# Performance work log

Measured on AMD Instinct MI355X. Metric: run time of the kernel, lower is better.

Reference implementation:

```python
import jax, jax.numpy as jnp
import numpy as np
import math

B, S, HID = 4, 1024, 1024
NH, HD = 16, 64  # CONSTANT_ATTENTION_HEAD_SIZE = 64
MAX_POS = 1024
LN_EPS = 1e-12


def setup_inputs() -> dict:
    key = jax.random.key(0)
    ks = jax.random.split(key, 12)
    sc = 0.02
    return {
        "hidden_states": jax.random.normal(ks[0], (B, S, HID), jnp.float32),
        "attention_mask": jnp.zeros((B, 1, 1, S), jnp.float32),
        "Wq": jax.random.normal(ks[1], (NH * HD, HID), jnp.float32) * sc,
        "bq": jnp.zeros((NH * HD,), jnp.float32),
        "Wk": jax.random.normal(ks[2], (NH * HD, HID), jnp.float32) * sc,
        "bk": jnp.zeros((NH * HD,), jnp.float32),
        "Wv": jax.random.normal(ks[3], (NH * HD, HID), jnp.float32) * sc,
        "bv": jnp.zeros((NH * HD,), jnp.float32),
        "dist_emb": jax.random.normal(ks[4], (2 * MAX_POS - 1, HD), jnp.float32) * sc,
        "Wo": jax.random.normal(ks[5], (HID, NH * HD), jnp.float32) * sc,
        "bo": jnp.zeros((HID,), jnp.float32),
        "ln_g": jnp.ones((HID,), jnp.float32),
        "ln_b": jnp.zeros((HID,), jnp.float32),
    }


def _heads(x):  # [B,S,NH*HD] -> [B,NH,S,HD]
    return x.reshape(B, S, NH, HD).transpose(0, 2, 1, 3)


def reference(hidden_states, attention_mask, Wq, bq, Wk, bk, Wv, bv,
              dist_emb, Wo, bo, ln_g, ln_b):
    q = _heads(hidden_states @ Wq.T + bq)
    k = _heads(hidden_states @ Wk.T + bk)
    v = _heads(hidden_states @ Wv.T + bv)

    # raw QK^T scores [B,NH,S,S]
    scores = jnp.einsum('bhld,bhrd->bhlr', q, k)

    # relative_key_query positional bias
    pos = jnp.arange(S)
    distance = pos[:, None] - pos[None, :] + MAX_POS - 1  # [S,S] in [0, 2*MAX_POS-2]
    pe = dist_emb[distance]  # [S,S,HD]
    scores = scores \
        + jnp.einsum('bhld,lrd->bhlr', q, pe) \
        + jnp.einsum('bhrd,lrd->bhlr', k, pe)

    scores = scores / math.sqrt(HD) + attention_mask
    probs = jax.nn.softmax(scores, axis=-1)

    ctx = jnp.einsum('bhlr,bhrd->bhld', probs, v)
    ctx = ctx.transpose(0, 2, 1, 3).reshape(B, S, NH * HD)

    # BertSelfOutputEx: dense + residual + LayerNorm (grow mask all ones, inactive)
    h = ctx @ Wo.T + bo + hidden_states
    mu = jnp.mean(h, axis=-1, keepdims=True)
    var = jnp.mean(jnp.square(h - mu), axis=-1, keepdims=True)
    out = (h - mu) * jax.lax.rsqrt(var + LN_EPS) * ln_g + ln_b
    return out
```

## Files before the change

kernel.cpp:

```cpp
#include <hip/hip_runtime.h>
#include <math.h>

#define BB   4
#define SS   1024
#define HIDD 1024
#define NHH  16
#define HDD  64

typedef short  short8 __attribute__((ext_vector_type(8)));
typedef float  f32x4  __attribute__((ext_vector_type(4)));

__device__ inline unsigned short f2bf(float f) {
    unsigned int u = __float_as_uint(f);
    u = (u + 0x7FFFu + ((u >> 16) & 1u)) >> 16;
    return (unsigned short)u;
}
__device__ inline float bf2f(unsigned short h) {
    return __uint_as_float(((unsigned int)h) << 16);
}

__global__ __launch_bounds__(256)
void conv_f2b(const float* __restrict__ s, unsigned short* __restrict__ d, int n)
{
    int i = (blockIdx.x * 256 + threadIdx.x) * 8;
    if (i >= n) return;
    float4 a = *(const float4*)&s[i];
    float4 b = *(const float4*)&s[i + 4];
    short8 o;
    o[0]=f2bf(a.x); o[1]=f2bf(a.y); o[2]=f2bf(a.z); o[3]=f2bf(a.w);
    o[4]=f2bf(b.x); o[5]=f2bf(b.y); o[6]=f2bf(b.z); o[7]=f2bf(b.w);
    *(short8*)&d[i] = o;
}

__global__ __launch_bounds__(256)
void conv_w(const float* __restrict__ wq, const float* __restrict__ wk,
            const float* __restrict__ wv, const float* __restrict__ wo,
            unsigned short* __restrict__ d)
{
    int i = (blockIdx.x * 256 + threadIdx.x) * 8;
    const float* s; int off;
    if      (i < 1048576)  { s = wq; off = i; }
    else if (i < 2097152)  { s = wk; off = i - 1048576; }
    else if (i < 3145728)  { s = wv; off = i - 2097152; }
    else                   { s = wo; off = i - 3145728; }
    float4 a = *(const float4*)&s[off];
    float4 b = *(const float4*)&s[off + 4];
    short8 o;
    o[0]=f2bf(a.x); o[1]=f2bf(a.y); o[2]=f2bf(a.z); o[3]=f2bf(a.w);
    o[4]=f2bf(b.x); o[5]=f2bf(b.y); o[6]=f2bf(b.z); o[7]=f2bf(b.w);
    *(short8*)&d[i] = o;
}

__global__ __launch_bounds__(256)
void conv_de(const float* __restrict__ s, unsigned short* __restrict__ d)
{
    int i = (blockIdx.x * 256 + threadIdx.x) * 8;
    short8 o;
    if (i < 131008) {
        float4 a = *(const float4*)&s[i];
        float4 b = *(const float4*)&s[i + 4];
        o[0]=f2bf(a.x); o[1]=f2bf(a.y); o[2]=f2bf(a.z); o[3]=f2bf(a.w);
        o[4]=f2bf(b.x); o[5]=f2bf(b.y); o[6]=f2bf(b.z); o[7]=f2bf(b.w);
    } else {
        o = (short8)0;
    }
    *(short8*)&d[i] = o;
}

__global__ __launch_bounds__(256)
void gemm_bf16(const unsigned short* __restrict__ A,
               const unsigned short* __restrict__ W,
               const float* __restrict__ bias0, const float* __restrict__ bias1,
               const float* __restrict__ bias2, const float* __restrict__ resid,
               unsigned short* __restrict__ oq, unsigned short* __restrict__ ok,
               unsigned short* __restrict__ ov, float* __restrict__ oc, int mode)
{
    __shared__ unsigned short A_l[128][40];
    __shared__ unsigned short B_l[128][40];

    const int tid = threadIdx.x;
    const int lane = tid & 63, w = tid >> 6;
    const int g = lane >> 4, x = lane & 15;
    const int m0 = blockIdx.x * 128;

    int sel = 0, n0;
    const unsigned short* Wp;
    if (mode == 1) { sel = blockIdx.y >> 3; n0 = (blockIdx.y & 7) * 128;
                     Wp = W + (size_t)sel * 1048576; }
    else           { n0 = blockIdx.y * 128; Wp = W; }

    f32x4 acc[4][4];
#pragma unroll
    for (int i = 0; i < 4; ++i)
#pragma unroll
        for (int j = 0; j < 4; ++j) acc[i][j] = (f32x4){0.f, 0.f, 0.f, 0.f};

    const int srow = tid >> 2, sc8 = (tid & 3) * 8;
    const unsigned short* Ap = A  + (size_t)(m0 + srow) * 1024 + sc8;
    const unsigned short* Bp = Wp + (size_t)(n0 + srow) * 1024 + sc8;

    short8 ra0 = *(const short8*)(Ap);
    short8 ra1 = *(const short8*)(Ap + 64 * 1024);
    short8 rb0 = *(const short8*)(Bp);
    short8 rb1 = *(const short8*)(Bp + 64 * 1024);

    const int mo = (w >> 1) * 64, no = (w & 1) * 64;
    const int fcol = g * 8;

    for (int ks = 0; ks < 32; ++ks) {
        __syncthreads();
        *(short8*)&A_l[srow     ][sc8] = ra0;
        *(short8*)&A_l[srow + 64][sc8] = ra1;
        *(short8*)&B_l[srow     ][sc8] = rb0;
        *(short8*)&B_l[srow + 64][sc8] = rb1;
        __syncthreads();
        if (ks < 31) {
            int k0 = (ks + 1) * 32;
            ra0 = *(const short8*)(Ap + k0);
            ra1 = *(const short8*)(Ap + 64 * 1024 + k0);
            rb0 = *(const short8*)(Bp + k0);
            rb1 = *(const short8*)(Bp + 64 * 1024 + k0);
        }
        short8 af[4], bf[4];
#pragma unroll
        for (int mi = 0; mi < 4; ++mi)
            af[mi] = *(const short8*)&A_l[mo + 16 * mi + x][fcol];
#pragma unroll
        for (int ni = 0; ni < 4; ++ni)
            bf[ni] = *(const short8*)&B_l[no + 16 * ni + x][fcol];
#pragma unroll
        for (int mi = 0; mi < 4; ++mi)
#pragma unroll
            for (int ni = 0; ni < 4; ++ni)
                acc[mi][ni] = __builtin_amdgcn_mfma_f32_16x16x32_bf16(
                    af[mi], bf[ni], acc[mi][ni], 0, 0, 0);
    }

    if (mode == 0) {
#pragma unroll
        for (int mi = 0; mi < 4; ++mi)
#pragma unroll
            for (int reg = 0; reg < 4; ++reg) {
                int m = m0 + mo + 16 * mi + g * 4 + reg;
#pragma unroll
                for (int ni = 0; ni < 4; ++ni) {
                    int n = n0 + no + 16 * ni + x;
                    oc[(size_t)m * 1024 + n] =
                        acc[mi][ni][reg] + bias0[n] + resid[(size_t)m * 1024 + n];
                }
            }
    } else {
        const float* bias = (sel == 0) ? bias0 : (sel == 1) ? bias1 : bias2;
        unsigned short* op = (sel == 0) ? oq : (sel == 1) ? ok : ov;
#pragma unroll
        for (int mi = 0; mi < 4; ++mi)
#pragma unroll
            for (int reg = 0; reg < 4; ++reg) {
                int m = m0 + mo + 16 * mi + g * 4 + reg;
                int b = m >> 10, s = m & 1023;
#pragma unroll
                for (int ni = 0; ni < 4; ++ni) {
                    int n = n0 + no + 16 * ni + x;
                    int h = n >> 6, d = n & 63;
                    op[((size_t)(b * NHH + h) * SS + s) * HDD + d] =
                        f2bf(acc[mi][ni][reg] + bias[n]);
                }
            }
    }
}

__global__ __launch_bounds__(256)
void vtrans(const unsigned short* __restrict__ vi, unsigned short* __restrict__ vo)
{
    __shared__ unsigned short t[64][72];
    const int tid = threadIdx.x;
    const int s0 = blockIdx.x * 64, bh = blockIdx.y;
    const unsigned short* src = vi + (size_t)bh * SS * HDD;
    unsigned short* dst = vo + (size_t)bh * SS * HDD;
#pragma unroll
    for (int c = 0; c < 2; ++c) {
        int idx = tid + 256 * c, row = idx >> 3, c8 = (idx & 7) * 8;
        *(short8*)&t[row][c8] = *(const short8*)&src[(size_t)(s0 + row) * 64 + c8];
    }
    __syncthreads();
#pragma unroll
    for (int c = 0; c < 2; ++c) {
        int idx = tid + 256 * c, d = idx >> 3, s8 = (idx & 7) * 8;
        short8 o;
#pragma unroll
        for (int j = 0; j < 8; ++j) o[j] = t[s8 + j][d];
        *(short8*)&dst[(size_t)d * 1024 + s0 + s8] = o;
    }
}

__global__ __launch_bounds__(256, 2)
void attn_mfma(const unsigned short* __restrict__ qg,
               const unsigned short* __restrict__ kg,
               const unsigned short* __restrict__ vtg,
               const float* __restrict__ mask,
               const unsigned short* __restrict__ de,
               unsigned short* __restrict__ ctx)
{
    __shared__ unsigned short Q_s [64][72];
    __shared__ unsigned short K_s [64][72];
    __shared__ unsigned short Vt_s[64][72];
    __shared__ unsigned short QPE_s[128][66];
    __shared__ unsigned short KPE_s[128][66];
    __shared__ unsigned short P_s [64][72];
    __shared__ float mask_s[64];

    const int tid = threadIdx.x;
    const int w = tid >> 6, lane = tid & 63;
    const int g = lane >> 4, x = lane & 15;
    const int l0 = blockIdx.x * 64, bh = blockIdx.y;
    const int b = bh >> 4, h = bh & 15;

    const unsigned short* qb = qg  + (size_t)bh * SS * HDD;
    const unsigned short* kb = kg  + (size_t)bh * SS * HDD;
    const unsigned short* vb = vtg + (size_t)bh * SS * HDD;

#pragma unroll
    for (int c = 0; c < 2; ++c) {
        int idx = tid + 256 * c, row = idx >> 3, c8 = (idx & 7) * 8;
        *(short8*)&Q_s[row][c8] = *(const short8*)&qb[(size_t)(l0 + row) * 64 + c8];
    }
    __syncthreads();

    short8 qf[4][2];
#pragma unroll
    for (int lf = 0; lf < 4; ++lf)
#pragma unroll
        for (int ks = 0; ks < 2; ++ks)
            qf[lf][ks] = *(const short8*)&Q_s[16 * lf + x][g * 8 + 32 * ks];

    f32x4 cacc[4];
#pragma unroll
    for (int i = 0; i < 4; ++i) cacc[i] = (f32x4){0.f, 0.f, 0.f, 0.f};
    float m_run = -1e30f, l_run = 0.f;
    const int lcol = 16 * w + x;

    for (int rt = 0; rt < 16; ++rt) {
        const int r0 = rt * 64;
        __syncthreads();
#pragma unroll
        for (int c = 0; c < 2; ++c) {
            int idx = tid + 256 * c, row = idx >> 3, c8 = (idx & 7) * 8;
            *(short8*)&K_s [row][c8] = *(const short8*)&kb[(size_t)(r0 + row) * 64 + c8];
            *(short8*)&Vt_s[row][c8] = *(const short8*)&vb[(size_t)row * 1024 + r0 + c8];
        }
        if (tid < 16) *(float4*)&mask_s[tid * 4] =
            *(const float4*)&mask[b * SS + r0 + tid * 4];
        __syncthreads();

        short8 kf[4][2];
#pragma unroll
        for (int rf = 0; rf < 4; ++rf)
#pragma unroll
            for (int ks = 0; ks < 2; ++ks)
                kf[rf][ks] = *(const short8*)&K_s[16 * rf + x][g * 8 + 32 * ks];

        f32x4 sacc[4];
#pragma unroll
        for (int i = 0; i < 4; ++i) sacc[i] = (f32x4){0.f, 0.f, 0.f, 0.f};
#pragma unroll
        for (int rf = 0; rf < 4; ++rf)
#pragma unroll
            for (int ks = 0; ks < 2; ++ks)
                sacc[rf] = __builtin_amdgcn_mfma_f32_16x16x32_bf16(
                    kf[rf][ks], qf[w][ks], sacc[rf], 0, 0, 0);

        const int t0 = l0 - r0 + 960;
        f32x4 qpe[2][4], kpe[2][4];
#pragma unroll
        for (int i = 0; i < 2; ++i)
#pragma unroll
            for (int j = 0; j < 4; ++j) {
                qpe[i][j] = (f32x4){0.f, 0.f, 0.f, 0.f};
                kpe[i][j] = (f32x4){0.f, 0.f, 0.f, 0.f};
            }
#pragma unroll
        for (int tf = 0; tf < 2; ++tf)
#pragma unroll
            for (int ks = 0; ks < 2; ++ks) {
                short8 pf = *(const short8*)&de[
                    (size_t)(t0 + 32 * w + 16 * tf + x) * 64 + g * 8 + 32 * ks];
#pragma unroll
                for (int lf = 0; lf < 4; ++lf)
                    qpe[tf][lf] = __builtin_amdgcn_mfma_f32_16x16x32_bf16(
                        pf, qf[lf][ks], qpe[tf][lf], 0, 0, 0);
#pragma unroll
                for (int rf = 0; rf < 4; ++rf)
                    kpe[tf][rf] = __builtin_amdgcn_mfma_f32_16x16x32_bf16(
                        pf, kf[rf][ks], kpe[tf][rf], 0, 0, 0);
            }
#pragma unroll
        for (int tf = 0; tf < 2; ++tf)
#pragma unroll
            for (int j = 0; j < 4; ++j)
#pragma unroll
                for (int reg = 0; reg < 4; ++reg) {
                    int t = 32 * w + 16 * tf + g * 4 + reg;
                    QPE_s[t][16 * j + x] = f2bf(qpe[tf][j][reg]);
                    KPE_s[t][16 * j + x] = f2bf(kpe[tf][j][reg]);
                }
        __syncthreads();

        float sc[4][4];
        float rmax = -1e30f;
#pragma unroll
        for (int fr = 0; fr < 4; ++fr)
#pragma unroll
            for (int reg = 0; reg < 4; ++reg) {
                int rr = 16 * fr + g * 4 + reg;
                int tl = lcol - rr + 63;
                float v = (sacc[fr][reg] + bf2f(QPE_s[tl][lcol])
                           + bf2f(KPE_s[tl][rr])) * 0.125f + mask_s[rr];
                sc[fr][reg] = v;
                rmax = fmaxf(rmax, v);
            }
        rmax = fmaxf(rmax, __shfl_xor(rmax, 16));
        rmax = fmaxf(rmax, __shfl_xor(rmax, 32));
        float mn = fmaxf(m_run, rmax);
        float rs = 0.f;
        float pr[4][4];
#pragma unroll
        for (int fr = 0; fr < 4; ++fr)
#pragma unroll
            for (int reg = 0; reg < 4; ++reg) {
                float p = __expf(sc[fr][reg] - mn);
                pr[fr][reg] = p; rs += p;
            }
        rs += __shfl_xor(rs, 16);
        rs += __shfl_xor(rs, 32);
        float fsc = __expf(m_run - mn);
        l_run = l_run * fsc + rs;
        m_run = mn;
#pragma unroll
        for (int fr = 0; fr < 4; ++fr) {
            uint2 pu;
            pu.x = (unsigned int)f2bf(pr[fr][0]) | ((unsigned int)f2bf(pr[fr][1]) << 16);
            pu.y = (unsigned int)f2bf(pr[fr][2]) | ((unsigned int)f2bf(pr[fr][3]) << 16);
            *(uint2*)&P_s[lcol][16 * fr + 4 * g] = pu;
        }
        __syncthreads();

        float fr4[4];
#pragma unroll
        for (int reg = 0; reg < 4; ++reg)
            fr4[reg] = __shfl(fsc, (g << 4) + (g << 2) + reg);
#pragma unroll
        for (int df = 0; df < 4; ++df)
#pragma unroll
            for (int reg = 0; reg < 4; ++reg)
                cacc[df][reg] *= fr4[reg];

        short8 pa[2];
#pragma unroll
        for (int ks = 0; ks < 2; ++ks)
            pa[ks] = *(const short8*)&P_s[16 * w + x][g * 8 + 32 * ks];
#pragma unroll
        for (int df = 0; df < 4; ++df)
#pragma unroll
            for (int ks = 0; ks < 2; ++ks) {
                short8 vf = *(const short8*)&Vt_s[16 * df + x][g * 8 + 32 * ks];
                cacc[df] = __builtin_amdgcn_mfma_f32_16x16x32_bf16(
                    pa[ks], vf, cacc[df], 0, 0, 0);
            }
    }

    float inv4[4];
#pragma unroll
    for (int reg = 0; reg < 4; ++reg)
        inv4[reg] = 1.f / __shfl(l_run, (g << 4) + (g << 2) + reg);
#pragma unroll
    for (int df = 0; df < 4; ++df)
#pragma unroll
        for (int reg = 0; reg < 4; ++reg) {
            int s = l0 + 16 * w + 4 * g + reg;
            int d = 16 * df + x;
            ctx[((size_t)(b * SS + s) * HIDD) + h * HDD + d] =
                f2bf(cacc[df][reg] * inv4[reg]);
        }
}

__global__ __launch_bounds__(256)
void ln_out(const float* __restrict__ hin, const float* __restrict__ g,
            const float* __restrict__ be, float* __restrict__ out)
{
    __shared__ float ssum[4], ssq[4];
    const int row = blockIdx.x;
    const int tid = threadIdx.x;
    float4 x = *(const float4*)&hin[(size_t)row * HIDD + 4 * tid];
    float sum = x.x + x.y + x.z + x.w;
    float sq  = x.x*x.x + x.y*x.y + x.z*x.z + x.w*x.w;
#pragma unroll
    for (int msk = 1; msk < 64; msk <<= 1) {
        sum += __shfl_xor(sum, msk);
        sq  += __shfl_xor(sq,  msk);
    }
    if ((tid & 63) == 0) { ssum[tid >> 6] = sum; ssq[tid >> 6] = sq; }
    __syncthreads();
    sum = ssum[0] + ssum[1] + ssum[2] + ssum[3];
    sq  = ssq[0]  + ssq[1]  + ssq[2]  + ssq[3];
    float mu  = sum * (1.f / 1024.f);
    float var = sq * (1.f / 1024.f) - mu * mu;
    float inv = rsqrtf(var + 1e-12f);
    float4 gv  = *(const float4*)&g[4 * tid];
    float4 bvv = *(const float4*)&be[4 * tid];
    float4 o;
    o.x = (x.x - mu) * inv * gv.x + bvv.x;
    o.y = (x.y - mu) * inv * gv.y + bvv.y;
    o.z = (x.z - mu) * inv * gv.z + bvv.z;
    o.w = (x.w - mu) * inv * gv.w + bvv.w;
    *(float4*)&out[(size_t)row * HIDD + 4 * tid] = o;
}

extern "C" void kernel_launch(void* const* d_in, const int* in_sizes, int n_in,
                              void* d_out, int out_size, void* d_ws, size_t ws_size,
                              hipStream_t stream)
{
    const float* hid  = (const float*)d_in[0];
    const float* mask = (const float*)d_in[1];
    const float* Wq   = (const float*)d_in[2];
    const float* bq   = (const float*)d_in[3];
    const float* Wk   = (const float*)d_in[4];
    const float* bk   = (const float*)d_in[5];
    const float* Wv   = (const float*)d_in[6];
    const float* bv   = (const float*)d_in[7];
    const float* de   = (const float*)d_in[8];
    const float* Wo   = (const float*)d_in[9];
    const float* bo   = (const float*)d_in[10];
    const float* lng  = (const float*)d_in[11];
    const float* lnb  = (const float*)d_in[12];
    float* out = (float*)d_out;

    unsigned short* hid_bf  = (unsigned short*)d_ws;
    unsigned short* wqkv_bf = hid_bf  + 4194304;
    unsigned short* wo_bf   = wqkv_bf + 3145728;
    unsigned short* de_bf   = wo_bf   + 1048576;
    unsigned short* q_bf    = de_bf   + 131072;
    unsigned short* k_bf    = q_bf    + 4194304;
    unsigned short* v_bf    = k_bf    + 4194304;
    unsigned short* vt_bf   = v_bf    + 4194304;
    unsigned short* ctx_bf  = vt_bf   + 4194304;
    float*          h_f     = (float*)q_bf;

    conv_f2b<<<2048, 256, 0, stream>>>(hid, hid_bf, 4194304);
    conv_w  <<<2048, 256, 0, stream>>>(Wq, Wk, Wv, Wo, wqkv_bf);
    conv_de <<<64,   256, 0, stream>>>(de, de_bf);

    gemm_bf16<<<dim3(32, 24), 256, 0, stream>>>(hid_bf, wqkv_bf, bq, bk, bv,
                                                nullptr, q_bf, k_bf, v_bf,
                                                nullptr, 1);
    vtrans<<<dim3(16, 64), 256, 0, stream>>>(v_bf, vt_bf);
    attn_mfma<<<dim3(16, 64), 256, 0, stream>>>(q_bf, k_bf, vt_bf, mask, de_bf,
                                                ctx_bf);
    gemm_bf16<<<dim3(32, 8), 256, 0, stream>>>(ctx_bf, wo_bf, bo, nullptr, nullptr,
                                               hid, nullptr, nullptr, nullptr,
                                               h_f, 0);
    ln_out<<<4096, 256, 0, stream>>>(h_f, lng, lnb, out);
}
```

Before: 318.3 us.

## Prefetch K/V tiles into registers, scatter bias into packed LDS, truncate bf16

The attention kernel now loads the next K, V-transposed and mask tile into registers while the current tile computes, which overlaps global loads with MFMA work. The QPE/KPE diagonal buffers are replaced by one packed BIAS[l][r] array, so each score reads both bias terms with a single 32-bit LDS load. LDS padding shrinks and launch bounds rise to 3 blocks per SM for more occupancy. bf16 conversion of the bias and probabilities now truncates instead of rounding, which adds some rounding error and register pressure from the prefetch registers.

Result: slower. 948.8 us (+198.1%).

```diff
diff --git a/kernel.cpp b/kernel.cpp
--- a/kernel.cpp
+++ b/kernel.cpp
@@ -17,6 +17,9 @@
 }
 __device__ inline float bf2f(unsigned short h) {
     return __uint_as_float(((unsigned int)h) << 16);
+}
+__device__ inline unsigned short f2bf_t(float f) {
+    return (unsigned short)(__float_as_uint(f) >> 16);
 }
 
 __global__ __launch_bounds__(256)
@@ -193,7 +196,7 @@
     }
 }
 
-__global__ __launch_bounds__(256, 2)
+__global__ __launch_bounds__(256, 3)
 void attn_mfma(const unsigned short* __restrict__ qg,
                const unsigned short* __restrict__ kg,
                const unsigned short* __restrict__ vtg,
@@ -201,12 +204,11 @@
                const unsigned short* __restrict__ de,
                unsigned short* __restrict__ ctx)
 {
-    __shared__ unsigned short Q_s [64][72];
-    __shared__ unsigned short K_s [64][72];
-    __shared__ unsigned short Vt_s[64][72];
-    __shared__ unsigned short QPE_s[128][66];
-    __shared__ unsigned short KPE_s[128][66];
-    __shared__ unsigned short P_s [64][72];
+    __shared__ unsigned short Q_s [64][68];
+    __shared__ unsigned short K_s [64][68];
+    __shared__ unsigned short Vt_s[64][68];
+    __shared__ unsigned short P_s [64][68];
+    __shared__ unsigned short BIAS[64][138];
     __shared__ float mask_s[64];
 
     const int tid = threadIdx.x;
@@ -239,18 +241,37 @@
     float m_run = -1e30f, l_run = 0.f;
     const int lcol = 16 * w + x;
 
+    short8 kr[2], vr[2];
+    float4 mr;
+#pragma unroll
+    for (int c = 0; c < 2; ++c) {
+        int idx = tid + 256 * c, row = idx >> 3, c8 = (idx & 7) * 8;
+        kr[c] = *(const short8*)&kb[(size_t)row * 64 + c8];
+        vr[c] = *(const short8*)&vb[(size_t)row * 1024 + c8];
+    }
+    mr = *(const float4*)&mask[b * SS + (tid & 15) * 4];
+
     for (int rt = 0; rt < 16; ++rt) {
-        const int r0 = rt * 64;
         __syncthreads();
 #pragma unroll
         for (int c = 0; c < 2; ++c) {
             int idx = tid + 256 * c, row = idx >> 3, c8 = (idx & 7) * 8;
-            *(short8*)&K_s [row][c8] = *(const short8*)&kb[(size_t)(r0 + row) * 64 + c8];
-            *(short8*)&Vt_s[row][c8] = *(const short8*)&vb[(size_t)row * 1024 + r0 + c8];
+            *(short8*)&K_s [row][c8] = kr[c];
+            *(short8*)&Vt_s[row][c8] = vr[c];
         }
-        if (tid < 16) *(float4*)&mask_s[tid * 4] =
-            *(const float4*)&mask[b * SS + r0 + tid * 4];
-        __syncthreads();
+        if (tid < 16) *(float4*)&mask_s[tid * 4] = mr;
+        __syncthreads();
+
+        {
+            int rn = ((rt + 1) & 15) * 64;
+#pragma unroll
+            for (int c = 0; c < 2; ++c) {
+                int idx = tid + 256 * c, row = idx >> 3, c8 = (idx & 7) * 8;
+                kr[c] = *(const short8*)&kb[(size_t)(rn + row) * 64 + c8];
+                vr[c] = *(const short8*)&vb[(size_t)row * 1024 + rn + c8];
+            }
+            mr = *(const float4*)&mask[b * SS + rn + (tid & 15) * 4];
+        }
 
         short8 kf[4][2];
 #pragma unroll
@@ -269,6 +290,7 @@
                 sacc[rf] = __builtin_amdgcn_mfma_f32_16x16x32_bf16(
                     kf[rf][ks], qf[w][ks], sacc[rf], 0, 0, 0);
 
+        const int r0 = rt * 64;
         const int t0 = l0 - r0 + 960;
         f32x4 qpe[2][4], kpe[2][4];
 #pragma unroll
@@ -296,13 +318,20 @@
 #pragma unroll
         for (int tf = 0; tf < 2; ++tf)
 #pragma unroll
-            for (int j = 0; j < 4; ++j)
-#pragma unroll
-                for (int reg = 0; reg < 4; ++reg) {
-                    int t = 32 * w + 16 * tf + g * 4 + reg;
-                    QPE_s[t][16 * j + x] = f2bf(qpe[tf][j][reg]);
-                    KPE_s[t][16 * j + x] = f2bf(kpe[tf][j][reg]);
+            for (int reg = 0; reg < 4; ++reg) {
+                int t = 32 * w + 16 * tf + 4 * g + reg;
+#pragma unroll
+                for (int j = 0; j < 4; ++j) {
+                    int lq = 16 * j + x;
+                    int rq = lq - t + 63;
+                    if ((unsigned)rq < 64u)
+                        BIAS[lq][2 * rq] = f2bf_t(qpe[tf][j][reg]);
+                    int rk = 16 * j + x;
+                    int lk = t + rk - 63;
+                    if ((unsigned)lk < 64u)
+                        BIAS[lk][2 * rk + 1] = f2bf_t(kpe[tf][j][reg]);
                 }
+            }
         __syncthreads();
 
         float sc[4][4];
@@ -311,10 +340,11 @@
         for (int fr = 0; fr < 4; ++fr)
 #pragma unroll
             for (int reg = 0; reg < 4; ++reg) {
-                int rr = 16 * fr + g * 4 + reg;
-                int tl = lcol - rr + 63;
-                float v = (sacc[fr][reg] + bf2f(QPE_s[tl][lcol])
-                           + bf2f(KPE_s[tl][rr])) * 0.125f + mask_s[rr];
+                int rr = 16 * fr + 4 * g + reg;
+                unsigned int pq = *(const unsigned int*)&BIAS[lcol][2 * rr];
+                float qv = __uint_as_float(pq << 16);
+                float kv = __uint_as_float(pq & 0xffff0000u);
+                float v = (sacc[fr][reg] + qv + kv) * 0.125f + mask_s[rr];
                 sc[fr][reg] = v;
                 rmax = fmaxf(rmax, v);
             }
@@ -338,8 +368,10 @@
 #pragma unroll
         for (int fr = 0; fr < 4; ++fr) {
             uint2 pu;
-            pu.x = (unsigned int)f2bf(pr[fr][0]) | ((unsigned int)f2bf(pr[fr][1]) << 16);
-            pu.y = (unsigned int)f2bf(pr[fr][2]) | ((unsigned int)f2bf(pr[fr][3]) << 16);
+            pu.x = __builtin_amdgcn_perm(__float_as_uint(pr[fr][1]),
+                                         __float_as_uint(pr[fr][0]), 0x07060302u);
+            pu.y = __builtin_amdgcn_perm(__float_as_uint(pr[fr][3]),
+                                         __float_as_uint(pr[fr][2]), 0x07060302u);
             *(uint2*)&P_s[lcol][16 * fr + 4 * g] = pu;
         }
         __syncthreads();
```
